# Performance work log

Measured on AMD Instinct MI355X. Metric: run time of the kernel, lower is better.

## Reference

```python
import jax, jax.numpy as jnp
import numpy as np

B, T, H, V = 16, 400, 400, 22000
S, STEPS, NG = 30, 8, 3  # n_slots, max_res_len, n_gates


def setup_inputs() -> dict:
    key = jax.random.key(0)
    ks = jax.random.split(key, 12)
    r = lambda k, shape, s: jax.random.normal(k, shape, jnp.float32) * s
    lens = jnp.sort(jax.random.randint(ks[8], (B,), T // 2, T + 1))[::-1]
    lens = lens.at[0].set(T)  # torch code only masks up to max(lens); make max(lens)==T
    return {
        "embedding": r(ks[0], (V, H), 0.1),
        "gru_Wih": r(ks[1], (3 * H, H), 0.05),
        "gru_Whh": r(ks[2], (3 * H, H), 0.05),
        "gru_bih": jnp.zeros((3 * H,), jnp.float32),
        "gru_bhh": jnp.zeros((3 * H,), jnp.float32),
        "W_ratio": r(ks[3], (1, 3 * H), 0.05),
        "b_ratio": jnp.zeros((1,), jnp.float32),
        "W_gate": r(ks[4], (NG, H), 0.05),
        "b_gate": jnp.zeros((NG,), jnp.float32),
        "slot_embs": r(ks[5], (S, H), 0.1),  # domain_emb + slot_emb, precombined per domain-slot
        "encoded_hidden": r(ks[6], (B, H), 1.0),
        "encoded_outputs": r(ks[7], (B, T, H), 1.0),
        "encoded_lens": lens,
        "story": jax.random.randint(ks[9], (B, T), 0, V),
        "target_batches": jax.random.randint(ks[10], (B, S, STEPS), 0, V),
    }


def reference(embedding, gru_Wih, gru_Whh, gru_bih, gru_bhh, W_ratio, b_ratio,
              W_gate, b_gate, slot_embs, encoded_hidden, encoded_outputs,
              encoded_lens, story, target_batches):
    # dropout is identity at eval; use_teacher_forcing=True.
    mask = jnp.arange(T)[None, :] < encoded_lens[:, None]          # [B, T]
    batch_idx = jnp.arange(B)[:, None]

    def gru_cell(x, h):
        gi = x @ gru_Wih.T + gru_bih                                # [B, 3H]
        gh = h @ gru_Whh.T + gru_bhh
        i_r, i_z, i_n = jnp.split(gi, 3, axis=-1)
        h_r, h_z, h_n = jnp.split(gh, 3, axis=-1)
        r = jax.nn.sigmoid(i_r + h_r)
        z = jax.nn.sigmoid(i_z + h_z)
        n = jnp.tanh(i_n + r * h_n)
        return (1.0 - z) * n + z * h

    def per_slot(slot_emb, tgt_steps):  # slot_emb [H], tgt_steps [STEPS, B]
        dec_in0 = jnp.broadcast_to(slot_emb[None, :], (B, H))

        def step(carry, tgt_w):
            h, dec_in = carry
            h = gru_cell(dec_in, h)                                 # dec_state == new hidden
            logits = jnp.einsum('bth,bh->bt', encoded_outputs, h)   # [B, T]
            attn = jax.nn.softmax(jnp.where(mask, logits, -1e9), axis=1)
            context = jnp.einsum('bt,bth->bh', attn, encoded_outputs)
            p_vocab = jax.nn.softmax(h @ embedding.T, axis=1)       # [B, V]
            pg_in = jnp.concatenate([h, context, dec_in], axis=-1)  # [B, 3H]
            p_gen = jax.nn.sigmoid(pg_in @ W_ratio.T + b_ratio)     # [B, 1]
            p_ctx = jnp.zeros((B, V), p_vocab.dtype).at[batch_idx, story].add(attn)
            p_final = (1.0 - p_gen) * p_ctx + p_gen * p_vocab       # [B, V]
            dec_next = embedding[tgt_w]                             # teacher forcing
            return (h, dec_next), (p_final, context)

        _, (points, contexts) = jax.lax.scan(step, (encoded_hidden, dec_in0), tgt_steps)
        gate = contexts[0] @ W_gate.T + b_gate                      # gate uses step-0 context
        return jnp.transpose(points, (1, 0, 2)), gate               # [B, STEPS, V], [B, NG]

    targets = jnp.transpose(target_batches, (1, 2, 0))              # [S, STEPS, B]
    all_point_outputs, all_gate_outputs = jax.vmap(per_slot)(slot_embs, targets)
    return all_point_outputs, all_gate_outputs  # [S,B,STEPS,V], [S,B,NG]
```

## Files before the change

kernel.cpp:

```cpp
#include <hip/hip_runtime.h>

#define DEV __device__ __forceinline__

constexpr int B = 16, T = 400, H = 400, V = 22000, S = 30, STEPS = 8, NG = 3;
constexpr int M  = S * B;
constexpr int H3 = 3 * H;
constexpr int KP = 416;
constexpr int VP = 22016;
constexpr int MP = 512;
constexpr int MR = STEPS * MP;
constexpr int NWP = 1280;
constexpr int NBLK = VP / 128;
constexpr int NMP = MR / 256;
constexpr int NVB = NBLK * NMP;
constexpr int TPAD = 416;
constexpr int PLD = 424;
constexpr long long PTS = (long long)S * B * STEPS * V;

typedef __attribute__((ext_vector_type(8))) short bfrag;
typedef __attribute__((ext_vector_type(4))) float f32x4;
typedef unsigned short u16;

DEV u16 f2bf(float x) {
  unsigned u = __float_as_uint(x);
  u += 0x7FFFu + ((u >> 16) & 1u);
  return (u16)(u >> 16);
}
DEV float bf2f(u16 h) { return __uint_as_float(((unsigned)h) << 16); }
DEV float sigm(float x) { return 1.0f / (1.0f + __expf(-x)); }

DEV void gload16(const u16* g, u16* l) {
  __builtin_amdgcn_global_load_lds(
      (const __attribute__((address_space(1))) void*)g,
      (__attribute__((address_space(3))) void*)l, 16, 0, 0);
}


__global__ void k_convert_emb(const float* __restrict__ emb, u16* __restrict__ ebf) {
  int i = blockIdx.x * 256 + threadIdx.x;
  if (i >= VP * KP) return;
  int v = i / KP, k = i % KP;
  float val = (v < V && k < H) ? emb[(long long)v * H + k] : 0.f;
  ebf[i] = f2bf(val);
}

__global__ void k_build_enc(const float* __restrict__ enc,
                            u16* __restrict__ encbK, u16* __restrict__ encT) {
  int i = blockIdx.x * 256 + threadIdx.x;
  if (i >= B * 400 * TPAD) return;
  int c = i % TPAD, r = (i / TPAD) % 400, b = i / (TPAD * 400);
  float v1 = (c < H) ? enc[((size_t)b * T + r) * H + c] : 0.f;
  encbK[i] = f2bf(v1);
  float v2 = (c < T) ? enc[((size_t)b * T + c) * H + r] : 0.f;
  encT[i] = f2bf(v2);
}

__global__ void k_convert_w(const float* __restrict__ Wih, const float* __restrict__ Whh,
                            u16* __restrict__ wihH, u16* __restrict__ wihL,
                            u16* __restrict__ whhH, u16* __restrict__ whhL) {
  int i = blockIdx.x * 256 + threadIdx.x;
  if (i >= NWP * KP) return;
  int n = i / KP, k = i % KP;
  float v1 = (n < H3 && k < H) ? Wih[n * H + k] : 0.f;
  u16 h1 = f2bf(v1);
  wihH[i] = h1; wihL[i] = f2bf(v1 - bf2f(h1));
  float v2 = (n < H3 && k < H) ? Whh[n * H + k] : 0.f;
  u16 h2 = f2bf(v2);
  whhH[i] = h2; whhL[i] = f2bf(v2 - bf2f(h2));
}

__global__ void k_init_dec(const float* __restrict__ emb, const float* __restrict__ semb,
                           const int* __restrict__ tgt, float* __restrict__ dec,
                           u16* __restrict__ dH, u16* __restrict__ dL) {
  int i = blockIdx.x * 256 + threadIdx.x;
  if (i >= STEPS * MP * KP) return;
  int k = i % KP, m = (i / KP) % MP, s = i / (KP * MP);
  float val = 0.f;
  if (m < M && k < H) {
    int slot = m / B, b = m % B;
    if (s == 0) val = semb[slot * H + k];
    else        val = emb[(long long)tgt[(b * S + slot) * STEPS + (s - 1)] * H + k];
    dec[((long long)s * M + m) * H + k] = val;
  }
  u16 hi = f2bf(val);
  dH[i] = hi; dL[i] = f2bf(val - bf2f(hi));
}

__global__ void k_init_h(const float* __restrict__ ehid, float* __restrict__ h0F,
                         u16* __restrict__ hH, u16* __restrict__ hL) {
  int i = blockIdx.x * 256 + threadIdx.x;
  if (i >= MP * KP) return;
  int k = i % KP, m = i / KP;
  float val = (m < M && k < H) ? ehid[(m % B) * H + k] : 0.f;
  if (m < M && k < H) h0F[m * H + k] = val;
  u16 hi = f2bf(val);
  hH[i] = hi; hL[i] = f2bf(val - bf2f(hi));
}

__global__ void k_zero_pad(u16* __restrict__ hAllH, u16* __restrict__ hAllL) {
  int i = blockIdx.x * 256 + threadIdx.x;
  if (i >= STEPS * (MP - M) * KP) return;
  int k = i % KP;
  int row = M + (i / KP) % (MP - M);
  int s = i / (KP * (MP - M));
  size_t idx = ((size_t)s * MP + row) * KP + k;
  hAllH[idx] = 0; hAllL[idx] = 0;
}

__global__ __launch_bounds__(256) void k_gemm64s(
    const u16* __restrict__ Ahi, const u16* __restrict__ Alo,
    const u16* __restrict__ Bmh, const u16* __restrict__ Bml,
    const float* __restrict__ bias, float* __restrict__ C,
    int Mvalid, int Nvalid, int Cstride)
{
  __shared__ u16 BsH[64 * 32], BsL[64 * 32];
  const int tid = threadIdx.x;
  const int wave = tid >> 6, lane = tid & 63;
  const int wm = wave >> 1, wn = wave & 1;
  const int n0 = blockIdx.x * 64;
  const int m0 = blockIdx.y * 64;
  const int lrow = lane & 15;
  const int c16 = lane >> 4;
  const int srow = tid >> 2;
  const int sg = (tid & 3) ^ (srow & 3);
  f32x4 acc[2][2] = {};

  const u16* aH = Ahi + (size_t)(m0 + wm * 32 + lrow) * KP + c16 * 8;
  const u16* aL = Alo + (size_t)(m0 + wm * 32 + lrow) * KP + c16 * 8;
  const u16* bHs = Bmh + (size_t)(n0 + srow) * KP + sg * 8;
  const u16* bLs = Bml + (size_t)(n0 + srow) * KP + sg * 8;
  u16* lBH = BsH + wave * 512;
  u16* lBL = BsL + wave * 512;

  for (int kk = 0; kk < KP / 32; ++kk) {
    const int kb = kk * 32;
    gload16(bHs + kb, lBH);
    gload16(bLs + kb, lBL);
    __syncthreads();
    bfrag a0h = *(const bfrag*)(aH + kb);
    bfrag a1h = *(const bfrag*)(aH + 16 * KP + kb);
    bfrag a0l = *(const bfrag*)(aL + kb);
    bfrag a1l = *(const bfrag*)(aL + 16 * KP + kb);
#pragma unroll
    for (int nn = 0; nn < 2; ++nn) {
      const int br = wn * 32 + nn * 16 + lrow;
      const int goff = br * 32 + ((c16 ^ (br & 3)) << 3);
      bfrag bh = *(const bfrag*)&BsH[goff];
      bfrag bl = *(const bfrag*)&BsL[goff];
      acc[0][nn] = __builtin_amdgcn_mfma_f32_16x16x32_bf16(a0h, bh, acc[0][nn], 0, 0, 0);
      acc[1][nn] = __builtin_amdgcn_mfma_f32_16x16x32_bf16(a1h, bh, acc[1][nn], 0, 0, 0);
      acc[0][nn] = __builtin_amdgcn_mfma_f32_16x16x32_bf16(a0h, bl, acc[0][nn], 0, 0, 0);
      acc[1][nn] = __builtin_amdgcn_mfma_f32_16x16x32_bf16(a1h, bl, acc[1][nn], 0, 0, 0);
      acc[0][nn] = __builtin_amdgcn_mfma_f32_16x16x32_bf16(a0l, bh, acc[0][nn], 0, 0, 0);
      acc[1][nn] = __builtin_amdgcn_mfma_f32_16x16x32_bf16(a1l, bh, acc[1][nn], 0, 0, 0);
    }
    __syncthreads();
  }
  const int orow = (lane >> 4) << 2, ocol = lane & 15;
#pragma unroll
  for (int am = 0; am < 2; ++am) {
#pragma unroll
    for (int nn = 0; nn < 2; ++nn) {
      const int gn = n0 + wn * 32 + nn * 16 + ocol;
      if (gn >= Nvalid) continue;
      const float badd = bias[gn];
#pragma unroll
      for (int r = 0; r < 4; ++r) {
        const int gm = m0 + wm * 32 + am * 16 + orow + r;
        if (gm < Mvalid) C[(long long)gm * Cstride + gn] = acc[am][nn][r] + badd;
      }
    }
  }
}

__global__ __launch_bounds__(512) void k_cell(const float* __restrict__ gi_s,
                                              const float* __restrict__ gh,
                                              const float* __restrict__ hprevF,
                                              float* __restrict__ hcurF,
                                              u16* __restrict__ hHc, u16* __restrict__ hLc) {
  int i = blockIdx.x * 512 + threadIdx.x;
  if (i >= M * H) return;
  int k = i % H, m = i / H;
  float ir = gi_s[m * H3 + k],         hr = gh[m * H3 + k];
  float iz = gi_s[m * H3 + H + k],     hz = gh[m * H3 + H + k];
  float in_ = gi_s[m * H3 + 2*H + k],  hn = gh[m * H3 + 2*H + k];
  float rr = sigm(ir + hr);
  float z = sigm(iz + hz);
  float n = tanhf(in_ + rr * hn);
  float hv = (1.f - z) * n + z * hprevF[i];
  hcurF[i] = hv;
  u16 hb = f2bf(hv);
  hHc[m * KP + k] = hb;
  hLc[m * KP + k] = f2bf(hv - bf2f(hb));
}

struct SMatt {
  u16 P[32 * PLD];
  float partm[32][4];
  float parts[32][4];
  float rowred[32];
  float part2[32][4][4];
};

__global__ __launch_bounds__(512) void k_attn(
    const u16* __restrict__ hAllH, const u16* __restrict__ hAllL,
    const float* __restrict__ hallF,
    const u16* __restrict__ encbK, const u16* __restrict__ encT,
    const int* __restrict__ lens, const float* __restrict__ dec,
    const float* __restrict__ Wr, const float* __restrict__ br,
    const float* __restrict__ Wg, const float* __restrict__ bg,
    float* __restrict__ attnB, float* __restrict__ pgenB, float* __restrict__ out)
{
  __shared__ SMatt sm;
  const int s = blockIdx.x >> 4;
  const int b = blockIdx.x & 15;
  const int tid = threadIdx.x;
  const int wave = tid >> 6, lane = tid & 63;
  const int mt = wave & 1;
  const int wg = wave >> 1;
  const int lrow = lane & 15;
  const int c16 = lane >> 4;
  const int len = lens[b];
  const int rbase = mt * 16 + c16 * 4;

  for (int idx = tid; idx < 32 * 24; idx += 512)
    sm.P[(idx / 24) * PLD + 400 + (idx % 24)] = 0;

  f32x4 acc[7] = {};
  {
    const size_t arow = (size_t)s * MP + (size_t)(mt * 16 + lrow) * B + b;
    const u16* aHp = hAllH + arow * KP + c16 * 8;
    const u16* aLp = hAllL + arow * KP + c16 * 8;
    const u16* bBase = encbK + (size_t)b * 400 * TPAD + c16 * 8;
    for (int kk = 0; kk < 13; ++kk) {
      bfrag ah = *(const bfrag*)(aHp + kk * 32);
      bfrag al = *(const bfrag*)(aLp + kk * 32);
#pragma unroll
      for (int i = 0; i < 7; ++i) {
        const int jt = wg + 4 * i;
        if (jt < 25) {
          bfrag bv = *(const bfrag*)(bBase + (size_t)(jt * 16 + lrow) * TPAD + kk * 32);
          acc[i] = __builtin_amdgcn_mfma_f32_16x16x32_bf16(ah, bv, acc[i], 0, 0, 0);
          acc[i] = __builtin_amdgcn_mfma_f32_16x16x32_bf16(al, bv, acc[i], 0, 0, 0);
        }
      }
    }
  }

  {
    float pm[4] = {-1e30f, -1e30f, -1e30f, -1e30f};
#pragma unroll
    for (int i = 0; i < 7; ++i) {
      const int jt = wg + 4 * i;
      if (jt >= 25) continue;
      const int t = jt * 16 + lrow;
      const bool ok = t < len;
#pragma unroll
      for (int rr = 0; rr < 4; ++rr) pm[rr] = fmaxf(pm[rr], ok ? acc[i][rr] : -1e30f);
    }
#pragma unroll
    for (int d = 1; d < 16; d <<= 1) {
#pragma unroll
      for (int rr = 0; rr < 4; ++rr) pm[rr] = fmaxf(pm[rr], __shfl_xor(pm[rr], d));
    }
    if (lrow == 0) {
#pragma unroll
      for (int rr = 0; rr < 4; ++rr) sm.partm[rbase + rr][wg] = pm[rr];
    }
  }
  __syncthreads();
  if (tid < 32)
    sm.rowred[tid] = fmaxf(fmaxf(sm.partm[tid][0], sm.partm[tid][1]),
                           fmaxf(sm.partm[tid][2], sm.partm[tid][3]));
  __syncthreads();
  float Mx[4];
#pragma unroll
  for (int rr = 0; rr < 4; ++rr) Mx[rr] = sm.rowred[rbase + rr];
  {
    float ps[4] = {0.f, 0.f, 0.f, 0.f};
#pragma unroll
    for (int i = 0; i < 7; ++i) {
      const int jt = wg + 4 * i;
      if (jt >= 25) continue;
      const int t = jt * 16 + lrow;
      const bool ok = t < len;
#pragma unroll
      for (int rr = 0; rr < 4; ++rr) {
        float e = ok ? __expf(acc[i][rr] - Mx[rr]) : 0.f;
        acc[i][rr] = e;
        ps[rr] += e;
      }
    }
#pragma unroll
    for (int d = 1; d < 16; d <<= 1) {
#pragma unroll
      for (int rr = 0; rr < 4; ++rr) ps[rr] += __shfl_xor(ps[rr], d);
    }
    if (lrow == 0) {
#pragma unroll
      for (int rr = 0; rr < 4; ++rr) sm.parts[rbase + rr][wg] = ps[rr];
    }
  }
  __syncthreads();
  if (tid < 32)
    sm.rowred[tid] = sm.parts[tid][0] + sm.parts[tid][1] + sm.parts[tid][2] + sm.parts[tid][3];
  __syncthreads();
  {
    float inv[4];
#pragma unroll
    for (int rr = 0; rr < 4; ++rr) inv[rr] = 1.f / sm.rowred[rbase + rr];
#pragma unroll
    for (int i = 0; i < 7; ++i) {
      const int jt = wg + 4 * i;
      if (jt >= 25) continue;
      const int t = jt * 16 + lrow;
#pragma unroll
      for (int rr = 0; rr < 4; ++rr) {
        const int row = rbase + rr;
        const float p = acc[i][rr] * inv[rr];
        sm.P[row * PLD + t] = f2bf(p);
        if (row < 30) attnB[((size_t)s * M + row * B + b) * T + t] = p;
      }
    }
  }
  __syncthreads();

  f32x4 acc2[7] = {};
  {
    const u16* bBase = encT + (size_t)b * 400 * TPAD + c16 * 8;
    const u16* aP = sm.P + (mt * 16 + lrow) * PLD + c16 * 8;
    for (int kk = 0; kk < 13; ++kk) {
      bfrag ap = *(const bfrag*)(aP + kk * 32);
#pragma unroll
      for (int i = 0; i < 7; ++i) {
        const int jk = wg + 4 * i;
        if (jk < 25) {
          bfrag bv = *(const bfrag*)(bBase + (size_t)(jk * 16 + lrow) * TPAD + kk * 32);
          acc2[i] = __builtin_amdgcn_mfma_f32_16x16x32_bf16(ap, bv, acc2[i], 0, 0, 0);
        }
      }
    }
  }
  {
    float pw[4] = {0.f, 0.f, 0.f, 0.f};
    float pg0[4] = {0.f, 0.f, 0.f, 0.f};
    float pg1[4] = {0.f, 0.f, 0.f, 0.f};
    float pg2[4] = {0.f, 0.f, 0.f, 0.f};
    const bool do_g = (s == 0);
#pragma unroll
    for (int i = 0; i < 7; ++i) {
      const int jk = wg + 4 * i;
      if (jk >= 25) continue;
      const int k = jk * 16 + lrow;
      const float wr = Wr[H + k];
      float w0 = 0.f, w1 = 0.f, w2 = 0.f;
      if (do_g) { w0 = Wg[k]; w1 = Wg[H + k]; w2 = Wg[2 * H + k]; }
#pragma unroll
      for (int rr = 0; rr < 4; ++rr) {
        const float v = acc2[i][rr];
        pw[rr] = fmaf(v, wr, pw[rr]);
        if (do_g) {
          pg0[rr] = fmaf(v, w0, pg0[rr]);
          pg1[rr] = fmaf(v, w1, pg1[rr]);
          pg2[rr] = fmaf(v, w2, pg2[rr]);
        }
      }
    }
#pragma unroll
    for (int d = 1; d < 16; d <<= 1) {
#pragma unroll
      for (int rr = 0; rr < 4; ++rr) {
        pw[rr] += __shfl_xor(pw[rr], d);
        pg0[rr] += __shfl_xor(pg0[rr], d);
        pg1[rr] += __shfl_xor(pg1[rr], d);
        pg2[rr] += __shfl_xor(pg2[rr], d);
      }
    }
    if (lrow == 0) {
#pragma unroll
      for (int rr = 0; rr < 4; ++rr) {
        sm.part2[rbase + rr][wg][0] = pw[rr];
        sm.part2[rbase + rr][wg][1] = pg0[rr];
        sm.part2[rbase + rr][wg][2] = pg1[rr];
        sm.part2[rbase + rr][wg][3] = pg2[rr];
      }
    }
  }
  __syncthreads();

  if (tid < 480) {
    const int row = tid >> 4;
    const int l16 = tid & 15;
    const int m = row * B + b;
    const float* hF = hallF + ((size_t)s * M + m) * H;
    const float* dF = dec + ((size_t)s * M + m) * H;
    float p = 0.f;
    for (int j = 0; j < 25; ++j) {
      const int k = l16 + 16 * j;
      p += hF[k] * Wr[k] + dF[k] * Wr[2 * H + k];
    }
#pragma unroll
    for (int d = 1; d < 16; d <<= 1) p += __shfl_xor(p, d);
    if (l16 == 0) {
      float cw = sm.part2[row][0][0] + sm.part2[row][1][0] +
                 sm.part2[row][2][0] + sm.part2[row][3][0];
      pgenB[s * M + m] = sigm(p + cw + br[0]);
    }
    if (s == 0 && l16 < NG) {
      float gv = sm.part2[row][0][1 + l16] + sm.part2[row][1][1 + l16] +
                 sm.part2[row][2][1 + l16] + sm.part2[row][3][1 + l16];
      out[PTS + (long long)m * NG + l16] = gv + bg[l16];
    }
  }
}

__global__ __launch_bounds__(512) void k_vocab(
    const u16* __restrict__ hAllH, const u16* __restrict__ ebf,
    u16* __restrict__ ebuf, float* __restrict__ pmax, float* __restrict__ psum)
{
  __shared__ u16 Bs[2 * 4096];
  __shared__ float lpm[256][2], lps[256][2], bmax[256];
  const int bx = blockIdx.x;
  const int tid = threadIdx.x;
  const int wave = tid >> 6, lane = tid & 63;
  const int bxs = (bx & 7) * (NVB / 8) + (bx >> 3);
  const int nb = bxs / NMP;
  const int mp = bxs % NMP;
  const int n0 = nb * 128;
  const int m0 = mp * 256;
  const int wm = wave >> 1, wn = wave & 1;
  const int lrow = lane & 15;
  const int c16 = lane >> 4;
  const int srow = tid >> 2;
  const int sg = (tid & 3) ^ (srow & 3);
  f32x4 acc[4][4] = {};

  const u16* aBase = hAllH + (size_t)(m0 + wm * 64 + lrow) * KP + c16 * 8;
  const u16* bS = ebf + (size_t)(n0 + srow) * KP + sg * 8;
  u16* lB0 = Bs + wave * 512;
  u16* lB1 = Bs + 4096 + wave * 512;

  gload16(bS, lB0);
  int cur = 0;
#pragma unroll 1
  for (int kk = 0; kk < 13; ++kk) {
    bfrag af0 = *(const bfrag*)(aBase + 0 * 16 * KP + kk * 32);
    bfrag af1 = *(const bfrag*)(aBase + 1 * 16 * KP + kk * 32);
    bfrag af2 = *(const bfrag*)(aBase + 2 * 16 * KP + kk * 32);
    bfrag af3 = *(const bfrag*)(aBase + 3 * 16 * KP + kk * 32);
    if (kk < 12) {
      gload16(bS + (kk + 1) * 32, cur ? lB0 : lB1);
      asm volatile("s_waitcnt vmcnt(5)" ::: "memory");
    } else {
      asm volatile("s_waitcnt vmcnt(4)" ::: "memory");
    }
    __builtin_amdgcn_sched_barrier(0);
    __builtin_amdgcn_s_barrier();
    const u16* Bb = Bs + (cur ? 4096 : 0);
    bfrag bfv[4];
#pragma unroll
    for (int nn = 0; nn < 4; ++nn) {
      const int brr = wn * 64 + nn * 16 + lrow;
      bfv[nn] = *(const bfrag*)&Bb[brr * 32 + ((c16 ^ (brr & 3)) << 3)];
    }
#pragma unroll
    for (int nn = 0; nn < 4; ++nn) {
      acc[0][nn] = __builtin_amdgcn_mfma_f32_16x16x32_bf16(af0, bfv[nn], acc[0][nn], 0, 0, 0);
      acc[1][nn] = __builtin_amdgcn_mfma_f32_16x16x32_bf16(af1, bfv[nn], acc[1][nn], 0, 0, 0);
      acc[2][nn] = __builtin_amdgcn_mfma_f32_16x16x32_bf16(af2, bfv[nn], acc[2][nn], 0, 0, 0);
      acc[3][nn] = __builtin_amdgcn_mfma_f32_16x16x32_bf16(af3, bfv[nn], acc[3][nn], 0, 0, 0);
    }
    __builtin_amdgcn_sched_barrier(0);
    __builtin_amdgcn_s_barrier();
    cur ^= 1;
  }
  __syncthreads();

  const int orow = (lane >> 4) << 2, ocol = lane & 15;
#pragma unroll
  for (int af_i = 0; af_i < 4; ++af_i) {
#pragma unroll
    for (int r = 0; r < 4; ++r) {
      float mxv = -1e30f;
#pragma unroll
      for (int nn = 0; nn < 4; ++nn) {
        const int gn = n0 + wn * 64 + nn * 16 + ocol;
        if (gn < V) mxv = fmaxf(mxv, acc[af_i][nn][r]);
      }
#pragma unroll
      for (int d = 1; d < 16; d <<= 1) mxv = fmaxf(mxv, __shfl_xor(mxv, d));
      if ((lane & 15) == 0) lpm[wm * 64 + af_i * 16 + orow + r][wn] = mxv;
    }
  }
  __syncthreads();
  if (tid < 256) bmax[tid] = fmaxf(lpm[tid][0], lpm[tid][1]);
  __syncthreads();
#pragma unroll
  for (int af_i = 0; af_i < 4; ++af_i) {
#pragma unroll
    for (int r = 0; r < 4; ++r) {
      const int rl = wm * 64 + af_i * 16 + orow + r;
      const int R = m0 + rl;
      const bool ok = (R % MP) < M;
      const float bm = bmax[rl];
      float se = 0.f;
#pragma unroll
      for (int nn = 0; nn < 4; ++nn) {
        const int gn = n0 + wn * 64 + nn * 16 + ocol;
        if (gn < V) {
          float e = __expf(acc[af_i][nn][r] - bm);
          se += e;
          if (ok) ebuf[(size_t)R * VP + gn] = f2bf(e);
        }
      }
#pragma unroll
      for (int d = 1; d < 16; d <<= 1) se += __shfl_xor(se, d);
      if ((lane & 15) == 0) lps[rl][wn] = se;
    }
  }
  __syncthreads();
  if (tid < 256) {
    const int R = m0 + tid;
    if ((R % MP) < M) {
      pmax[(size_t)R * NBLK + nb] = bmax[tid];
      psum[(size_t)R * NBLK + nb] = lps[tid][0] + lps[tid][1];
    }
  }
}

__global__ __launch_bounds__(512) void k_merge(
    const u16* __restrict__ ebuf, const float* __restrict__ pmax,
    const float* __restrict__ psum, const float* __restrict__ pgenB,
    const float* __restrict__ attnB, const int* __restrict__ story,
    float* __restrict__ out)
{
  const int bxi = blockIdx.x;
  const int s = bxi / M, m = bxi % M, b = m % B;
  const size_t R = (size_t)s * MP + m;
  const int tid = threadIdx.x;
  const int wave = tid >> 6, lane = tid & 63;
  __shared__ float fact[NBLK], red8[8];
  float pm = (tid < NBLK) ? pmax[R * NBLK + tid] : -1e30f;
  float wv = pm;
#pragma unroll
  for (int off = 32; off; off >>= 1) wv = fmaxf(wv, __shfl_xor(wv, off));
  if (lane == 0) red8[wave] = wv;
  __syncthreads();
  float Mx = red8[0];
#pragma unroll
  for (int j = 1; j < 8; ++j) Mx = fmaxf(Mx, red8[j]);
  __syncthreads();
  float sv = (tid < NBLK) ? psum[R * NBLK + tid] * __expf(pm - Mx) : 0.f;
  float ws = sv;
#pragma unroll
  for (int off = 32; off; off >>= 1) ws += __shfl_xor(ws, off);
  if (lane == 0) red8[wave] = ws;
  __syncthreads();
  float Sv = 0.f;
#pragma unroll
  for (int j = 0; j < 8; ++j) Sv += red8[j];
  const float pg = pgenB[s * M + m];
  const float scale = pg / Sv;
  if (tid < NBLK) fact[tid] = __expf(pm - Mx) * scale;
  __syncthreads();

  const u16* erow = ebuf + R * VP;
  float* orow = out + ((size_t)m * STEPS + s) * V;
  for (int v = tid; v < V; v += 512) orow[v] = bf2f(erow[v]) * fact[v >> 7];
  __syncthreads();
  const float om = 1.f - pg;
  for (int t = tid; t < T; t += 512) {
    float a = attnB[((size_t)s * M + m) * T + t];
    if (a != 0.f) atomicAdd(orow + story[b * T + t], om * a);
  }
}


extern "C" void kernel_launch(void* const* d_in, const int* in_sizes, int n_in,
                              void* d_out, int out_size, void* d_ws, size_t ws_size,
                              hipStream_t stream) {
  (void)in_sizes; (void)n_in; (void)out_size; (void)ws_size;
  const float* emb  = (const float*)d_in[0];
  const float* Wih  = (const float*)d_in[1];
  const float* Whh  = (const float*)d_in[2];
  const float* bih  = (const float*)d_in[3];
  const float* bhh  = (const float*)d_in[4];
  const float* Wr   = (const float*)d_in[5];
  const float* br   = (const float*)d_in[6];
  const float* Wg   = (const float*)d_in[7];
  const float* bg   = (const float*)d_in[8];
  const float* semb = (const float*)d_in[9];
  const float* ehid = (const float*)d_in[10];
  const float* enc  = (const float*)d_in[11];
  const int*   lens = (const int*)d_in[12];
  const int*   story= (const int*)d_in[13];
  const int*   tgt  = (const int*)d_in[14];
  float* out = (float*)d_out;

  char* w = (char*)d_ws;
  size_t off = 0;
  auto alloc = [&](size_t n) -> void* {
    void* p = w + off;
    off = (off + n + 255) & ~(size_t)255;
    return p;
  };
  u16* ebf    = (u16*)alloc((size_t)VP * KP * 2);
  u16* wihH   = (u16*)alloc((size_t)NWP * KP * 2);
  u16* wihL   = (u16*)alloc((size_t)NWP * KP * 2);
  u16* whhH   = (u16*)alloc((size_t)NWP * KP * 2);
  u16* whhL   = (u16*)alloc((size_t)NWP * KP * 2);
  u16* decH   = (u16*)alloc((size_t)STEPS * MP * KP * 2);
  u16* decL   = (u16*)alloc((size_t)STEPS * MP * KP * 2);
  float* dec  = (float*)alloc((size_t)STEPS * M * H * 4);
  float* h0F  = (float*)alloc((size_t)M * H * 4);
  u16* h0H    = (u16*)alloc((size_t)MP * KP * 2);
  u16* h0L    = (u16*)alloc((size_t)MP * KP * 2);
  u16* hAllH  = (u16*)alloc((size_t)MR * KP * 2);
  u16* hAllL  = (u16*)alloc((size_t)MR * KP * 2);
  float* hallF= (float*)alloc((size_t)STEPS * M * H * 4);
  float* gi   = (float*)alloc((size_t)STEPS * MP * H3 * 4);
  float* gh   = (float*)alloc((size_t)M * H3 * 4);
  float* attnB= (float*)alloc((size_t)STEPS * M * T * 4);
  float* pgenB= (float*)alloc((size_t)STEPS * M * 4);
  u16* ebuf   = (u16*)alloc((size_t)MR * VP * 2);
  float* pmx  = (float*)alloc((size_t)MR * NBLK * 4);
  float* psm  = (float*)alloc((size_t)MR * NBLK * 4);
  u16* encbK  = (u16*)alloc((size_t)B * 400 * TPAD * 2);
  u16* encT   = (u16*)alloc((size_t)B * 400 * TPAD * 2);

  k_convert_emb<<<VP * KP / 256, 256, 0, stream>>>(emb, ebf);
  k_build_enc<<<(B * 400 * TPAD + 255) / 256, 256, 0, stream>>>(enc, encbK, encT);
  k_convert_w<<<NWP * KP / 256, 256, 0, stream>>>(Wih, Whh, wihH, wihL, whhH, whhL);
  k_init_dec<<<STEPS * MP * KP / 256, 256, 0, stream>>>(emb, semb, tgt, dec, decH, decL);
  k_init_h<<<MP * KP / 256, 256, 0, stream>>>(ehid, h0F, h0H, h0L);
  k_zero_pad<<<(STEPS * (MP - M) * KP + 255) / 256, 256, 0, stream>>>(hAllH, hAllL);
  k_gemm64s<<<dim3((H3 + 63) / 64, MR / 64), 256, 0, stream>>>(
      decH, decL, wihH, wihL, bih, gi, MR, H3, H3);

  for (int s = 0; s < STEPS; ++s) {
    const u16* pH = (s == 0) ? h0H : hAllH + (size_t)(s - 1) * MP * KP;
    const u16* pL = (s == 0) ? h0L : hAllL + (size_t)(s - 1) * MP * KP;
    const float* pF = (s == 0) ? h0F : hallF + (size_t)(s - 1) * M * H;
    k_gemm64s<<<dim3((H3 + 63) / 64, (M + 63) / 64), 256, 0, stream>>>(
        pH, pL, whhH, whhL, bhh, gh, M, H3, H3);
    k_cell<<<(M * H + 511) / 512, 512, 0, stream>>>(
        gi + (size_t)s * MP * H3, gh, pF,
        hallF + (size_t)s * M * H,
        hAllH + (size_t)s * MP * KP, hAllL + (size_t)s * MP * KP);
  }

  k_attn<<<STEPS * B, 512, 0, stream>>>(hAllH, hAllL, hallF, encbK, encT, lens,
                                        dec, Wr, br, Wg, bg, attnB, pgenB, out);
  k_vocab<<<NVB, 512, 0, stream>>>(hAllH, ebf, ebuf, pmx, psm);
  k_merge<<<STEPS * M, 512, 0, stream>>>(ebuf, pmx, psm, pgenB, attnB, story, out);
}
```

Baseline: 646.6 us.

## Fuse init kernels, fuse GRU gemm with cell, drop max-subtraction in vocab softmax

Merges six setup kernels into one launch and fuses the recurrent Whh GEMM with the GRU cell update, so the gh buffer round trip and per-step launches go away. The vocab GEMM now uses 64-wide K tiles with an 8-way XOR swizzle, and KP grows to 448 to fit them. Vocab logits are exponentiated without per-block max subtraction, which removes the pmax/psum partials and lets the merge kernel sum bf16 exps directly. This relies on the logits staying small enough not to overflow exp, and it also changes the LDS swizzle, the bf16 rounding helper and the launch order.

```diff
diff --git a/kernel.cpp b/kernel.cpp
--- a/kernel.cpp
+++ b/kernel.cpp
@@ -1,11 +1,12 @@
 #include <hip/hip_runtime.h>
+#include <hip/hip_bf16.h>
 
 #define DEV __device__ __forceinline__
 
 constexpr int B = 16, T = 400, H = 400, V = 22000, S = 30, STEPS = 8, NG = 3;
 constexpr int M  = S * B;
 constexpr int H3 = 3 * H;
-constexpr int KP = 416;
+constexpr int KP = 448;
 constexpr int VP = 22016;
 constexpr int MP = 512;
 constexpr int MR = STEPS * MP;
@@ -26,6 +27,10 @@
   u += 0x7FFFu + ((u >> 16) & 1u);
   return (u16)(u >> 16);
 }
+DEV u16 f2bfn(float x) {
+  __hip_bfloat16 h = __float2bfloat16(x);
+  union { __hip_bfloat16 b; u16 u; } cv; cv.b = h; return cv.u;
+}
 DEV float bf2f(u16 h) { return __uint_as_float(((unsigned)h) << 16); }
 DEV float sigm(float x) { return 1.0f / (1.0f + __expf(-x)); }
 
@@ -35,76 +40,96 @@
       (__attribute__((address_space(3))) void*)l, 16, 0, 0);
 }
 
-
-__global__ void k_convert_emb(const float* __restrict__ emb, u16* __restrict__ ebf) {
-  int i = blockIdx.x * 256 + threadIdx.x;
-  if (i >= VP * KP) return;
-  int v = i / KP, k = i % KP;
-  float val = (v < V && k < H) ? emb[(long long)v * H + k] : 0.f;
-  ebf[i] = f2bf(val);
-}
-
-__global__ void k_build_enc(const float* __restrict__ enc,
-                            u16* __restrict__ encbK, u16* __restrict__ encT) {
-  int i = blockIdx.x * 256 + threadIdx.x;
-  if (i >= B * 400 * TPAD) return;
-  int c = i % TPAD, r = (i / TPAD) % 400, b = i / (TPAD * 400);
-  float v1 = (c < H) ? enc[((size_t)b * T + r) * H + c] : 0.f;
-  encbK[i] = f2bf(v1);
-  float v2 = (c < T) ? enc[((size_t)b * T + c) * H + r] : 0.f;
-  encT[i] = f2bf(v2);
-}
-
-__global__ void k_convert_w(const float* __restrict__ Wih, const float* __restrict__ Whh,
-                            u16* __restrict__ wihH, u16* __restrict__ wihL,
-                            u16* __restrict__ whhH, u16* __restrict__ whhL) {
-  int i = blockIdx.x * 256 + threadIdx.x;
-  if (i >= NWP * KP) return;
-  int n = i / KP, k = i % KP;
-  float v1 = (n < H3 && k < H) ? Wih[n * H + k] : 0.f;
-  u16 h1 = f2bf(v1);
-  wihH[i] = h1; wihL[i] = f2bf(v1 - bf2f(h1));
-  float v2 = (n < H3 && k < H) ? Whh[n * H + k] : 0.f;
-  u16 h2 = f2bf(v2);
-  whhH[i] = h2; whhL[i] = f2bf(v2 - bf2f(h2));
-}
-
-__global__ void k_init_dec(const float* __restrict__ emb, const float* __restrict__ semb,
-                           const int* __restrict__ tgt, float* __restrict__ dec,
-                           u16* __restrict__ dH, u16* __restrict__ dL) {
-  int i = blockIdx.x * 256 + threadIdx.x;
-  if (i >= STEPS * MP * KP) return;
-  int k = i % KP, m = (i / KP) % MP, s = i / (KP * MP);
-  float val = 0.f;
-  if (m < M && k < H) {
-    int slot = m / B, b = m % B;
-    if (s == 0) val = semb[slot * H + k];
-    else        val = emb[(long long)tgt[(b * S + slot) * STEPS + (s - 1)] * H + k];
-    dec[((long long)s * M + m) * H + k] = val;
-  }
-  u16 hi = f2bf(val);
-  dH[i] = hi; dL[i] = f2bf(val - bf2f(hi));
-}
-
-__global__ void k_init_h(const float* __restrict__ ehid, float* __restrict__ h0F,
-                         u16* __restrict__ hH, u16* __restrict__ hL) {
-  int i = blockIdx.x * 256 + threadIdx.x;
-  if (i >= MP * KP) return;
-  int k = i % KP, m = i / KP;
-  float val = (m < M && k < H) ? ehid[(m % B) * H + k] : 0.f;
-  if (m < M && k < H) h0F[m * H + k] = val;
-  u16 hi = f2bf(val);
-  hH[i] = hi; hL[i] = f2bf(val - bf2f(hi));
-}
-
-__global__ void k_zero_pad(u16* __restrict__ hAllH, u16* __restrict__ hAllL) {
-  int i = blockIdx.x * 256 + threadIdx.x;
-  if (i >= STEPS * (MP - M) * KP) return;
-  int k = i % KP;
-  int row = M + (i / KP) % (MP - M);
-  int s = i / (KP * (MP - M));
-  size_t idx = ((size_t)s * MP + row) * KP + k;
-  hAllH[idx] = 0; hAllL[idx] = 0;
+constexpr int N_EMB = VP * KP / 256;
+constexpr int N_ENC = B * 400 * TPAD / 256;
+constexpr int N_W   = NWP * KP / 256;
+constexpr int N_DEC = STEPS * MP * KP / 256;
+constexpr int N_H0  = MP * KP / 256;
+constexpr int N_ZP  = STEPS * (MP - M) * KP / 256;
+constexpr int N_ZE  = MR * 16 / 256;
+constexpr int N_INIT = N_EMB + N_ENC + N_W + N_DEC + N_H0 + N_ZP + N_ZE;
+
+__global__ __launch_bounds__(256) void k_init(
+    const float* __restrict__ emb, const float* __restrict__ enc,
+    const float* __restrict__ Wih, const float* __restrict__ Whh,
+    const float* __restrict__ semb, const float* __restrict__ ehid,
+    const int* __restrict__ tgt,
+    u16* __restrict__ ebf, u16* __restrict__ encbK, u16* __restrict__ encT,
+    u16* __restrict__ wihH, u16* __restrict__ wihL,
+    u16* __restrict__ whhH, u16* __restrict__ whhL,
+    float* __restrict__ dec, u16* __restrict__ decH, u16* __restrict__ decL,
+    float* __restrict__ h0F, u16* __restrict__ h0H, u16* __restrict__ h0L,
+    u16* __restrict__ hAllH, u16* __restrict__ hAllL, u16* __restrict__ ebuf)
+{
+  int bx = blockIdx.x;
+  const int tid = threadIdx.x;
+  if (bx < N_EMB) {
+    int i = bx * 256 + tid;
+    int v = i / KP, k = i % KP;
+    ebf[i] = f2bf((v < V && k < H) ? emb[(long long)v * H + k] : 0.f);
+    return;
+  }
+  bx -= N_EMB;
+  if (bx < N_ENC) {
+    int i = bx * 256 + tid;
+    int c = i % TPAD, r = (i / TPAD) % 400, b = i / (TPAD * 400);
+    encbK[i] = f2bf((c < H) ? enc[((size_t)b * T + r) * H + c] : 0.f);
+    encT[i]  = f2bf((c < T) ? enc[((size_t)b * T + c) * H + r] : 0.f);
+    return;
+  }
+  bx -= N_ENC;
+  if (bx < N_W) {
+    int i = bx * 256 + tid;
+    int n = i / KP, k = i % KP;
+    float v1 = (n < H3 && k < H) ? Wih[n * H + k] : 0.f;
+    u16 h1 = f2bf(v1);
+    wihH[i] = h1; wihL[i] = f2bf(v1 - bf2f(h1));
+    float v2 = (n < H3 && k < H) ? Whh[n * H + k] : 0.f;
+    u16 h2 = f2bf(v2);
+    whhH[i] = h2; whhL[i] = f2bf(v2 - bf2f(h2));
+    return;
+  }
+  bx -= N_W;
+  if (bx < N_DEC) {
+    int i = bx * 256 + tid;
+    int k = i % KP, m = (i / KP) % MP, s = i / (KP * MP);
+    float val = 0.f;
+    if (m < M && k < H) {
+      int slot = m / B, b = m % B;
+      if (s == 0) val = semb[slot * H + k];
+      else        val = emb[(long long)tgt[(b * S + slot) * STEPS + (s - 1)] * H + k];
+      dec[((long long)s * M + m) * H + k] = val;
+    }
+    u16 hi = f2bf(val);
+    decH[i] = hi; decL[i] = f2bf(val - bf2f(hi));
+    return;
+  }
+  bx -= N_DEC;
+  if (bx < N_H0) {
+    int i = bx * 256 + tid;
+    int k = i % KP, m = i / KP;
+    float val = (m < M && k < H) ? ehid[(m % B) * H + k] : 0.f;
+    if (m < M && k < H) h0F[m * H + k] = val;
+    u16 hi = f2bf(val);
+    h0H[i] = hi; h0L[i] = f2bf(val - bf2f(hi));
+    return;
+  }
+  bx -= N_H0;
+  if (bx < N_ZP) {
+    int i = bx * 256 + tid;
+    int k = i % KP;
+    int row = M + (i / KP) % (MP - M);
+    int s = i / (KP * (MP - M));
+    size_t idx = ((size_t)s * MP + row) * KP + k;
+    hAllH[idx] = 0; hAllL[idx] = 0;
+    return;
+  }
+  bx -= N_ZP;
+  {
+    int i = bx * 256 + tid;
+    int row = i / 16, col = V + (i % 16);
+    ebuf[(size_t)row * VP + col] = 0;
+  }
 }
 
 __global__ __launch_bounds__(256) void k_gemm64s(
@@ -122,7 +147,7 @@
   const int lrow = lane & 15;
   const int c16 = lane >> 4;
   const int srow = tid >> 2;
-  const int sg = (tid & 3) ^ (srow & 3);
+  const int sg = (tid & 3) ^ ((srow >> 1) & 3);
   f32x4 acc[2][2] = {};
 
   const u16* aH = Ahi + (size_t)(m0 + wm * 32 + lrow) * KP + c16 * 8;
@@ -144,7 +169,7 @@
 #pragma unroll
     for (int nn = 0; nn < 2; ++nn) {
       const int br = wn * 32 + nn * 16 + lrow;
-      const int goff = br * 32 + ((c16 ^ (br & 3)) << 3);
+      const int goff = br * 32 + ((c16 ^ ((br >> 1) & 3)) << 3);
       bfrag bh = *(const bfrag*)&BsH[goff];
       bfrag bl = *(const bfrag*)&BsL[goff];
       acc[0][nn] = __builtin_amdgcn_mfma_f32_16x16x32_bf16(a0h, bh, acc[0][nn], 0, 0, 0);
@@ -173,25 +198,86 @@
   }
 }
 
-__global__ __launch_bounds__(512) void k_cell(const float* __restrict__ gi_s,
-                                              const float* __restrict__ gh,
-                                              const float* __restrict__ hprevF,
-                                              float* __restrict__ hcurF,
-                                              u16* __restrict__ hHc, u16* __restrict__ hLc) {
-  int i = blockIdx.x * 512 + threadIdx.x;
-  if (i >= M * H) return;
-  int k = i % H, m = i / H;
-  float ir = gi_s[m * H3 + k],         hr = gh[m * H3 + k];
-  float iz = gi_s[m * H3 + H + k],     hz = gh[m * H3 + H + k];
-  float in_ = gi_s[m * H3 + 2*H + k],  hn = gh[m * H3 + 2*H + k];
-  float rr = sigm(ir + hr);
-  float z = sigm(iz + hz);
-  float n = tanhf(in_ + rr * hn);
-  float hv = (1.f - z) * n + z * hprevF[i];
-  hcurF[i] = hv;
-  u16 hb = f2bf(hv);
-  hHc[m * KP + k] = hb;
-  hLc[m * KP + k] = f2bf(hv - bf2f(hb));
+__global__ __launch_bounds__(256) void k_grustep(
+    const u16* __restrict__ hpH, const u16* __restrict__ hpL,
+    const float* __restrict__ hprevF,
+    const u16* __restrict__ whhH, const u16* __restrict__ whhL,
+    const float* __restrict__ bhh, const float* __restrict__ gi_s,
+    float* __restrict__ hcurF, u16* __restrict__ hcH, u16* __restrict__ hcL)
+{
+  __shared__ u16 BsH[3][64 * 32], BsL[3][64 * 32];
+  const int tid = threadIdx.x;
+  const int wave = tid >> 6, lane = tid & 63;
+  const int wm = wave >> 1, wn = wave & 1;
+  const int c0 = blockIdx.x * 64;
+  const int m0 = blockIdx.y * 64;
+  const int lrow = lane & 15;
+  const int c16 = lane >> 4;
+  const int srow = tid >> 2;
+  const int sg = (tid & 3) ^ ((srow >> 1) & 3);
+  f32x4 acc[3][2][2] = {};
+
+  const u16* aH = hpH + (size_t)(m0 + wm * 32 + lrow) * KP + c16 * 8;
+  const u16* aL = hpL + (size_t)(m0 + wm * 32 + lrow) * KP + c16 * 8;
+  const u16* bH0 = whhH + (size_t)(c0 + srow) * KP + sg * 8;
+  const u16* bL0 = whhL + (size_t)(c0 + srow) * KP + sg * 8;
+
+  for (int kk = 0; kk < KP / 32; ++kk) {
+    const int kb = kk * 32;
+#pragma unroll
+    for (int g = 0; g < 3; ++g) {
+      gload16(bH0 + (size_t)g * 400 * KP + kb, &BsH[g][wave * 512]);
+      gload16(bL0 + (size_t)g * 400 * KP + kb, &BsL[g][wave * 512]);
+    }
+    __syncthreads();
+    bfrag a0h = *(const bfrag*)(aH + kb);
+    bfrag a1h = *(const bfrag*)(aH + 16 * KP + kb);
+    bfrag a0l = *(const bfrag*)(aL + kb);
+    bfrag a1l = *(const bfrag*)(aL + 16 * KP + kb);
+#pragma unroll
+    for (int g = 0; g < 3; ++g) {
+#pragma unroll
+      for (int nn = 0; nn < 2; ++nn) {
+        const int br = wn * 32 + nn * 16 + lrow;
+        const int goff = br * 32 + ((c16 ^ ((br >> 1) & 3)) << 3);
+        bfrag bh = *(const bfrag*)&BsH[g][goff];
+        bfrag bl = *(const bfrag*)&BsL[g][goff];
+        acc[g][0][nn] = __builtin_amdgcn_mfma_f32_16x16x32_bf16(a0h, bh, acc[g][0][nn], 0, 0, 0);
+        acc[g][1][nn] = __builtin_amdgcn_mfma_f32_16x16x32_bf16(a1h, bh, acc[g][1][nn], 0, 0, 0);
+        acc[g][0][nn] = __builtin_amdgcn_mfma_f32_16x16x32_bf16(a0h, bl, acc[g][0][nn], 0, 0, 0);
+        acc[g][1][nn] = __builtin_amdgcn_mfma_f32_16x16x32_bf16(a1h, bl, acc[g][1][nn], 0, 0, 0);
+        acc[g][0][nn] = __builtin_amdgcn_mfma_f32_16x16x32_bf16(a0l, bh, acc[g][0][nn], 0, 0, 0);
+        acc[g][1][nn] = __builtin_amdgcn_mfma_f32_16x16x32_bf16(a1l, bh, acc[g][1][nn], 0, 0, 0);
+      }
+    }
+    __syncthreads();
+  }
+  const int orow = (lane >> 4) << 2, ocol = lane & 15;
+#pragma unroll
+  for (int am = 0; am < 2; ++am) {
+#pragma unroll
+    for (int nn = 0; nn < 2; ++nn) {
+      const int gk = c0 + wn * 32 + nn * 16 + ocol;
+      if (gk >= H) continue;
+      const float b0 = bhh[gk], b1 = bhh[H + gk], b2 = bhh[2 * H + gk];
+#pragma unroll
+      for (int r = 0; r < 4; ++r) {
+        const int gm = m0 + wm * 32 + am * 16 + orow + r;
+        if (gm >= M) continue;
+        float ir = gi_s[(size_t)gm * H3 + gk];
+        float iz = gi_s[(size_t)gm * H3 + H + gk];
+        float in_ = gi_s[(size_t)gm * H3 + 2 * H + gk];
+        float rr = sigm(ir + acc[0][am][nn][r] + b0);
+        float z  = sigm(iz + acc[1][am][nn][r] + b1);
+        float n  = tanhf(in_ + rr * (acc[2][am][nn][r] + b2));
+        float hv = (1.f - z) * n + z * hprevF[(size_t)gm * H + gk];
+        hcurF[(size_t)gm * H + gk] = hv;
+        u16 hb = f2bf(hv);
+        hcH[(size_t)gm * KP + gk] = hb;
+        hcL[(size_t)gm * KP + gk] = f2bf(hv - bf2f(hb));
+      }
+    }
+  }
 }
 
 struct SMatt {
@@ -318,7 +404,7 @@
       for (int rr = 0; rr < 4; ++rr) {
         const int row = rbase + rr;
         const float p = acc[i][rr] * inv[rr];
-        sm.P[row * PLD + t] = f2bf(p);
+        sm.P[row * PLD + t] = f2bfn(p);
         if (row < 30) attnB[((size_t)s * M + row * B + b) * T + t] = p;
       }
     }
@@ -416,10 +502,9 @@
 
 __global__ __launch_bounds__(512) void k_vocab(
     const u16* __restrict__ hAllH, const u16* __restrict__ ebf,
-    u16* __restrict__ ebuf, float* __restrict__ pmax, float* __restrict__ psum)
+    u16* __restrict__ ebuf)
 {
-  __shared__ u16 Bs[2 * 4096];
-  __shared__ float lpm[256][2], lps[256][2], bmax[256];
+  __shared__ u16 Bs[2][8192];
   const int bx = blockIdx.x;
   const int tid = threadIdx.x;
   const int wave = tid >> 6, lane = tid & 63;
@@ -431,106 +516,77 @@
   const int wm = wave >> 1, wn = wave & 1;
   const int lrow = lane & 15;
   const int c16 = lane >> 4;
-  const int srow = tid >> 2;
-  const int sg = (tid & 3) ^ (srow & 3);
+  const int sr0 = wave * 8 + (lane >> 3);
+  const int slot = lane & 7;
   f32x4 acc[4][4] = {};
 
   const u16* aBase = hAllH + (size_t)(m0 + wm * 64 + lrow) * KP + c16 * 8;
-  const u16* bS = ebf + (size_t)(n0 + srow) * KP + sg * 8;
-  u16* lB0 = Bs + wave * 512;
-  u16* lB1 = Bs + 4096 + wave * 512;
-
-  gload16(bS, lB0);
+  const u16* bS0 = ebf + (size_t)(n0 + sr0) * KP + (size_t)((slot ^ (sr0 & 7)) * 8);
+  const u16* bS1 = ebf + (size_t)(n0 + sr0 + 64) * KP + (size_t)((slot ^ ((sr0 + 64) & 7)) * 8);
+
+  gload16(bS0, &Bs[0][wave * 512]);
+  gload16(bS1, &Bs[0][4096 + wave * 512]);
   int cur = 0;
 #pragma unroll 1
-  for (int kk = 0; kk < 13; ++kk) {
-    bfrag af0 = *(const bfrag*)(aBase + 0 * 16 * KP + kk * 32);
-    bfrag af1 = *(const bfrag*)(aBase + 1 * 16 * KP + kk * 32);
-    bfrag af2 = *(const bfrag*)(aBase + 2 * 16 * KP + kk * 32);
-    bfrag af3 = *(const bfrag*)(aBase + 3 * 16 * KP + kk * 32);
-    if (kk < 12) {
-      gload16(bS + (kk + 1) * 32, cur ? lB0 : lB1);
-      asm volatile("s_waitcnt vmcnt(5)" ::: "memory");
+  for (int p = 0; p < 7; ++p) {
+    const int kb = p * 64;
+    bfrag a[4][2];
+#pragma unroll
+    for (int r = 0; r < 4; ++r) {
+      a[r][0] = *(const bfrag*)(aBase + r * 16 * KP + kb);
+      a[r][1] = *(const bfrag*)(aBase + r * 16 * KP + kb + 32);
+    }
+    if (p < 6) {
+      gload16(bS0 + kb + 64, &Bs[cur ^ 1][wave * 512]);
+      gload16(bS1 + kb + 64, &Bs[cur ^ 1][4096 + wave * 512]);
+      asm volatile("s_waitcnt vmcnt(10)" ::: "memory");
     } else {
-      asm volatile("s_waitcnt vmcnt(4)" ::: "memory");
+      asm volatile("s_waitcnt vmcnt(8)" ::: "memory");
     }
     __builtin_amdgcn_sched_barrier(0);
     __builtin_amdgcn_s_barrier();
-    const u16* Bb = Bs + (cur ? 4096 : 0);
-    bfrag bfv[4];
-#pragma unroll
-    for (int nn = 0; nn < 4; ++nn) {
-      const int brr = wn * 64 + nn * 16 + lrow;
-      bfv[nn] = *(const bfrag*)&Bb[brr * 32 + ((c16 ^ (brr & 3)) << 3)];
-    }
-#pragma unroll
-    for (int nn = 0; nn < 4; ++nn) {
-      acc[0][nn] = __builtin_amdgcn_mfma_f32_16x16x32_bf16(af0, bfv[nn], acc[0][nn], 0, 0, 0);
-      acc[1][nn] = __builtin_amdgcn_mfma_f32_16x16x32_bf16(af1, bfv[nn], acc[1][nn], 0, 0, 0);
-      acc[2][nn] = __builtin_amdgcn_mfma_f32_16x16x32_bf16(af2, bfv[nn], acc[2][nn], 0, 0, 0);
-      acc[3][nn] = __builtin_amdgcn_mfma_f32_16x16x32_bf16(af3, bfv[nn], acc[3][nn], 0, 0, 0);
+    const u16* Bb = Bs[cur];
+#pragma unroll
+    for (int ks = 0; ks < 2; ++ks) {
+      bfrag bfv[4];
+#pragma unroll
+      for (int nn = 0; nn < 4; ++nn) {
+        const int brr = wn * 64 + nn * 16 + lrow;
+        const int g = (ks * 4 + c16) ^ (brr & 7);
+        bfv[nn] = *(const bfrag*)&Bb[brr * 64 + g * 8];
+      }
+#pragma unroll
+      for (int nn = 0; nn < 4; ++nn) {
+#pragma unroll
+        for (int r = 0; r < 4; ++r)
+          acc[r][nn] = __builtin_amdgcn_mfma_f32_16x16x32_bf16(a[r][ks], bfv[nn], acc[r][nn], 0, 0, 0);
+      }
     }
     __builtin_amdgcn_sched_barrier(0);
     __builtin_amdgcn_s_barrier();
     cur ^= 1;
   }
-  __syncthreads();
 
   const int orow = (lane >> 4) << 2, ocol = lane & 15;
-#pragma unroll
-  for (int af_i = 0; af_i < 4; ++af_i) {
+  const int mbase = (m0 & 511);
+#pragma unroll
+  for (int af = 0; af < 4; ++af) {
 #pragma unroll
     for (int r = 0; r < 4; ++r) {
-      float mxv = -1e30f;
+      const int rl = wm * 64 + af * 16 + orow + r;
+      if (mbase + rl >= M && mbase + rl < MP) continue;
+      const size_t R = (size_t)m0 + rl;
 #pragma unroll
       for (int nn = 0; nn < 4; ++nn) {
         const int gn = n0 + wn * 64 + nn * 16 + ocol;
-        if (gn < V) mxv = fmaxf(mxv, acc[af_i][nn][r]);
-      }
-#pragma unroll
-      for (int d = 1; d < 16; d <<= 1) mxv = fmaxf(mxv, __shfl_xor(mxv, d));
-      if ((lane & 15) == 0) lpm[wm * 64 + af_i * 16 + orow + r][wn] = mxv;
-    }
-  }
-  __syncthreads();
-  if (tid < 256) bmax[tid] = fmaxf(lpm[tid][0], lpm[tid][1]);
-  __syncthreads();
-#pragma unroll
-  for (int af_i = 0; af_i < 4; ++af_i) {
-#pragma unroll
-    for (int r = 0; r < 4; ++r) {
-      const int rl = wm * 64 + af_i * 16 + orow + r;
-      const int R = m0 + rl;
-      const bool ok = (R % MP) < M;
-      const float bm = bmax[rl];
-      float se = 0.f;
-#pragma unroll
-      for (int nn = 0; nn < 4; ++nn) {
-        const int gn = n0 + wn * 64 + nn * 16 + ocol;
-        if (gn < V) {
-          float e = __expf(acc[af_i][nn][r] - bm);
-          se += e;
-          if (ok) ebuf[(size_t)R * VP + gn] = f2bf(e);
-        }
-      }
-#pragma unroll
-      for (int d = 1; d < 16; d <<= 1) se += __shfl_xor(se, d);
-      if ((lane & 15) == 0) lps[rl][wn] = se;
-    }
-  }
-  __syncthreads();
-  if (tid < 256) {
-    const int R = m0 + tid;
-    if ((R % MP) < M) {
-      pmax[(size_t)R * NBLK + nb] = bmax[tid];
-      psum[(size_t)R * NBLK + nb] = lps[tid][0] + lps[tid][1];
+        if (gn < V) ebuf[R * VP + gn] = f2bfn(__expf(acc[af][nn][r]));
+      }
     }
   }
 }
 
 __global__ __launch_bounds__(512) void k_merge(
-    const u16* __restrict__ ebuf, const float* __restrict__ pmax,
-    const float* __restrict__ psum, const float* __restrict__ pgenB,
+    const u16* __restrict__ ebuf, const float* __restrict__ pgenB,
     const float* __restrict__ attnB, const int* __restrict__ story,
     float* __restrict__ out)
 {
@@ -539,34 +595,43 @@
   const size_t R = (size_t)s * MP + m;
   const int tid = threadIdx.x;
   const int wave = tid >> 6, lane = tid & 63;
-  __shared__ float fact[NBLK], red8[8];
-  float pm = (tid < NBLK) ? pmax[R * NBLK + tid] : -1e30f;
-  float wv = pm;
-#pragma unroll
-  for (int off = 32; off; off >>= 1) wv = fmaxf(wv, __shfl_xor(wv, off));
-  if (lane == 0) red8[wave] = wv;
-  __syncthreads();
-  float Mx = red8[0];
-#pragma unroll
-  for (int j = 1; j < 8; ++j) Mx = fmaxf(Mx, red8[j]);
-  __syncthreads();
-  float sv = (tid < NBLK) ? psum[R * NBLK + tid] * __expf(pm - Mx) : 0.f;
-  float ws = sv;
-#pragma unroll
-  for (int off = 32; off; off >>= 1) ws += __shfl_xor(ws, off);
-  if (lane == 0) red8[wave] = ws;
+  __shared__ float red8[8];
+  const u16* erow = ebuf + R * VP;
+  bfrag ch[6];
+  float sum = 0.f;
+#pragma unroll
+  for (int j = 0; j < 6; ++j) {
+    const int c = j * 512 + tid;
+    if (c < VP / 8) {
+      ch[j] = *(const bfrag*)(erow + (size_t)c * 8);
+#pragma unroll
+      for (int e = 0; e < 8; ++e) sum += bf2f((u16)ch[j][e]);
+    }
+  }
+#pragma unroll
+  for (int off = 32; off; off >>= 1) sum += __shfl_xor(sum, off);
+  if (lane == 0) red8[wave] = sum;
   __syncthreads();
   float Sv = 0.f;
 #pragma unroll
   for (int j = 0; j < 8; ++j) Sv += red8[j];
   const float pg = pgenB[s * M + m];
   const float scale = pg / Sv;
-  if (tid < NBLK) fact[tid] = __expf(pm - Mx) * scale;
-  __syncthreads();
-
-  const u16* erow = ebuf + R * VP;
   float* orow = out + ((size_t)m * STEPS + s) * V;
-  for (int v = tid; v < V; v += 512) orow[v] = bf2f(erow[v]) * fact[v >> 7];
+#pragma unroll
+  for (int j = 0; j < 6; ++j) {
+    const int c = j * 512 + tid;
+    if (c < V / 8) {
+      f32x4 w0, w1;
+#pragma unroll
+      for (int e = 0; e < 4; ++e) {
+        w0[e] = bf2f((u16)ch[j][e]) * scale;
+        w1[e] = bf2f((u16)ch[j][4 + e]) * scale;
+      }
+      *(f32x4*)(orow + (size_t)c * 8) = w0;
+      *(f32x4*)(orow + (size_t)c * 8 + 4) = w1;
+    }
+  }
   __syncthreads();
   const float om = 1.f - pg;
   for (int t = tid; t < T; t += 512) {
@@ -618,22 +683,16 @@
   u16* hAllH  = (u16*)alloc((size_t)MR * KP * 2);
   u16* hAllL  = (u16*)alloc((size_t)MR * KP * 2);
   float* hallF= (float*)alloc((size_t)STEPS * M * H * 4);
-  float* gi   = (float*)alloc((size_t)STEPS * MP * H3 * 4);
-  float* gh   = (float*)alloc((size_t)M * H3 * 4);
+  float* gi   = (float*)alloc((size_t)MR * H3 * 4);
   float* attnB= (float*)alloc((size_t)STEPS * M * T * 4);
   float* pgenB= (float*)alloc((size_t)STEPS * M * 4);
   u16* ebuf   = (u16*)alloc((size_t)MR * VP * 2);
-  float* pmx  = (float*)alloc((size_t)MR * NBLK * 4);
-  float* psm  = (float*)alloc((size_t)MR * NBLK * 4);
   u16* encbK  = (u16*)alloc((size_t)B * 400 * TPAD * 2);
   u16* encT   = (u16*)alloc((size_t)B * 400 * TPAD * 2);
 
-  k_convert_emb<<<VP * KP / 256, 256, 0, stream>>>(emb, ebf);
-  k_build_enc<<<(B * 400 * TPAD + 255) / 256, 256, 0, stream>>>(enc, encbK, encT);
-  k_convert_w<<<NWP * KP / 256, 256, 0, stream>>>(Wih, Whh, wihH, wihL, whhH, whhL);
-  k_init_dec<<<STEPS * MP * KP / 256, 256, 0, stream>>>(emb, semb, tgt, dec, decH, decL);
-  k_init_h<<<MP * KP / 256, 256, 0, stream>>>(ehid, h0F, h0H, h0L);
-  k_zero_pad<<<(STEPS * (MP - M) * KP + 255) / 256, 256, 0, stream>>>(hAllH, hAllL);
+  k_init<<<N_INIT, 256, 0, stream>>>(emb, enc, Wih, Whh, semb, ehid, tgt,
+      ebf, encbK, encT, wihH, wihL, whhH, whhL, dec, decH, decL,
+      h0F, h0H, h0L, hAllH, hAllL, ebuf);
   k_gemm64s<<<dim3((H3 + 63) / 64, MR / 64), 256, 0, stream>>>(
       decH, decL, wihH, wihL, bih, gi, MR, H3, H3);
 
@@ -641,16 +700,14 @@
     const u16* pH = (s == 0) ? h0H : hAllH + (size_t)(s - 1) * MP * KP;
     const u16* pL = (s == 0) ? h0L : hAllL + (size_t)(s - 1) * MP * KP;
     const float* pF = (s == 0) ? h0F : hallF + (size_t)(s - 1) * M * H;
-    k_gemm64s<<<dim3((H3 + 63) / 64, (M + 63) / 64), 256, 0, stream>>>(
-        pH, pL, whhH, whhL, bhh, gh, M, H3, H3);
-    k_cell<<<(M * H + 511) / 512, 512, 0, stream>>>(
-        gi + (size_t)s * MP * H3, gh, pF,
+    k_grustep<<<dim3((H + 63) / 64, (M + 63) / 64), 256, 0, stream>>>(
+        pH, pL, pF, whhH, whhL, bhh, gi + (size_t)s * MP * H3,
         hallF + (size_t)s * M * H,
         hAllH + (size_t)s * MP * KP, hAllL + (size_t)s * MP * KP);
   }
 
+  k_vocab<<<NVB, 512, 0, stream>>>(hAllH, ebf, ebuf);
   k_attn<<<STEPS * B, 512, 0, stream>>>(hAllH, hAllL, hallF, encbK, encT, lens,
                                         dec, Wr, br, Wg, bg, attnB, pgenB, out);
-  k_vocab<<<NVB, 512, 0, stream>>>(hAllH, ebf, ebuf, pmx, psm);
-  k_merge<<<STEPS * M, 512, 0, stream>>>(ebuf, pmx, psm, pgenB, attnB, story, out);
-}
+  k_merge<<<STEPS * M, 512, 0, stream>>>(ebuf, pgenB, attnB, story, out);
+}
```

New measurement: 729.5 us. 1.13x slower.
